# Optimization experiments

Measured on AMD Instinct MI355X. Metric: run time of the kernel, lower is better.

## Reference

```python
import jax, jax.numpy as jnp
import numpy as np

B, C, H, W, NH = 8, 256, 32, 32, 4  # batch, channels, height, width, heads


def groupnorm(x, w, b, eps=1e-5):
    # GroupNorm with 1 group: normalize over (C,H,W) per sample
    mu = x.mean(axis=(1, 2, 3), keepdims=True)
    var = x.var(axis=(1, 2, 3), keepdims=True)
    xn = (x - mu) * jax.lax.rsqrt(var + eps)
    return xn * w[None, :, None, None] + b[None, :, None, None]


def setup_inputs() -> dict:
    key = jax.random.key(0)
    ks = jax.random.split(key, 6)
    C4 = 4 * C
    s = lambda k, shape, scale: jax.random.normal(k, shape, jnp.float32) * scale
    return {
        "x": jax.random.normal(ks[0], (B, C, H, W), jnp.float32),
        "qkv_w": s(ks[1], (3 * C, C), 0.05),   # 1x1 conv, no bias
        "uh_w": s(ks[2], (C, C), 0.05),
        "uh_b": jnp.zeros((C,), jnp.float32),
        "n1_w": jnp.ones((C,), jnp.float32),
        "n1_b": jnp.zeros((C,), jnp.float32),
        "n2_w": jnp.ones((C,), jnp.float32),
        "n2_b": jnp.zeros((C,), jnp.float32),
        "f1_w": s(ks[3], (C4, C), 0.05),
        "f1_b": jnp.zeros((C4,), jnp.float32),
        "f2_w": s(ks[4], (C, C4), 0.05),
        "f2_b": jnp.zeros((C,), jnp.float32),
        # torch inits these to 0; use nonzero values so both branches contribute
        "gamma_attn": jnp.array(0.5, jnp.float32),
        "gamma_ffn": jnp.array(0.5, jnp.float32),
    }


def reference(x, qkv_w, uh_w, uh_b, n1_w, n1_b, n2_w, n2_b,
              f1_w, f1_b, f2_w, f2_b, gamma_attn, gamma_ffn):
    Bx, Cx, Hx, Wx = x.shape
    N = Hx * Wx
    dk = Cx // NH
    # --- attention branch (eval mode: DropPath is identity) ---
    xn = groupnorm(x, n1_w, n1_b).reshape(Bx, Cx, N)
    qkv = jnp.einsum('oc,bcn->bon', qkv_w, xn)          # 1x1 conv == channel matmul
    q, k, v = [t.reshape(Bx, NH, dk, N) for t in jnp.split(qkv, 3, axis=1)]
    scores = jnp.einsum('bhdi,bhdj->bhij', q, k) / np.float32(np.sqrt(dk))
    attn = jax.nn.softmax(scores, axis=-1)               # [B,H,N,N]
    out = jnp.einsum('bhij,bhdj->bhdi', attn, v).reshape(Bx, Cx, N)
    uh = jnp.einsum('oc,bcn->bon', uh_w, out) + uh_b[None, :, None]
    x2 = x + gamma_attn * uh.reshape(Bx, Cx, Hx, Wx)
    # --- FFN branch ---
    h = groupnorm(x2, n2_w, n2_b).reshape(Bx, Cx, N)
    h = jax.nn.silu(jnp.einsum('oc,bcn->bon', f1_w, h) + f1_b[None, :, None])
    h = jnp.einsum('oc,bcn->bon', f2_w, h) + f2_b[None, :, None]
    return x2 + gamma_ffn * h.reshape(Bx, Cx, Hx, Wx)
```

## Files before the change

kernel.cpp:

```cpp
#include <hip/hip_runtime.h>
#include <math.h>

#define Bsz 8
#define Cch 256
#define Nsp 1024
#define NHd 4
#define QS  0.18033688011112042f

using bf16x8  = __attribute__((ext_vector_type(8))) short;
using f32x4   = __attribute__((ext_vector_type(4))) float;
using ushort8 = __attribute__((ext_vector_type(8))) unsigned short;
#define MFMA(a,b,c) __builtin_amdgcn_mfma_f32_16x16x32_bf16(a,b,c,0,0,0)

__device__ inline unsigned short f2bf(float f) {
    unsigned int u = __float_as_uint(f);
    u = u + 0x7fffu + ((u >> 16) & 1u);
    return (unsigned short)(u >> 16);
}
__device__ inline float bf2f(unsigned short u) {
    return __uint_as_float((unsigned int)u << 16);
}
__device__ inline unsigned int cvtpk(float lo, float hi) {
    unsigned int r;
    asm("v_cvt_pk_bf16_f32 %0, %1, %2" : "=v"(r) : "v"(lo), "v"(hi));
    return r;
}

__global__ __launch_bounds__(256) void wconv_gn(const float* __restrict__ a, const float* __restrict__ b,
                                                const float* __restrict__ c, const float* __restrict__ d,
                                                unsigned short* __restrict__ o,
                                                const float* __restrict__ x,
                                                float* __restrict__ part) {
    if (blockIdx.x < 3072) {
        size_t i = (size_t)blockIdx.x * 256 + threadIdx.x;
        float v;
        if (i < 196608) v = a[i];
        else if (i < 262144) v = b[i - 196608];
        else if (i < 524288) v = c[i - 262144];
        else v = d[i - 524288];
        o[i] = f2bf(v);
        return;
    }
    int blk = blockIdx.x - 3072;
    int bb = blk >> 6;
    const float* xb = x + (size_t)bb * (Cch * Nsp) + (size_t)(blk & 63) * 4096;
    int t = threadIdx.x;
    float s = 0.f, s2 = 0.f;
    for (int i = t; i < 4096; i += 256) { float v = xb[i]; s += v; s2 += v * v; }
    __shared__ float sh[256], sh2[256];
    sh[t] = s; sh2[t] = s2; __syncthreads();
    for (int off = 128; off; off >>= 1) {
        if (t < off) { sh[t] += sh[t + off]; sh2[t] += sh2[t + off]; }
        __syncthreads();
    }
    if (t == 0) { part[blk * 2] = sh[0]; part[blk * 2 + 1] = sh2[0]; }
}

__global__ __launch_bounds__(256) void gn_apply_t(const float* __restrict__ x,
                                                  const float* __restrict__ part, int npart,
                                                  const float* __restrict__ w,
                                                  const float* __restrict__ bb,
                                                  unsigned short* __restrict__ out_cl) {
    int b = blockIdx.z, c0 = blockIdx.y * 64, n0 = blockIdx.x * 64;
    __shared__ float tile[64][65];
    __shared__ float smu, srs;
    int t = threadIdx.x;
    if (t < 64) {
        float s = 0.f, s2 = 0.f;
        for (int u = t; u < npart; u += 64) {
            s += part[(b * npart + u) * 2]; s2 += part[(b * npart + u) * 2 + 1];
        }
        for (int m = 1; m < 64; m <<= 1) { s += __shfl_xor(s, m); s2 += __shfl_xor(s2, m); }
        if (t == 0) {
            float inv_n = 1.f / (Cch * Nsp);
            float mu = s * inv_n;
            float var = s2 * inv_n - mu * mu;
            smu = mu; srs = rsqrtf(var + 1e-5f);
        }
    }
    const float* xb = x + ((size_t)b * Cch + c0) * Nsp + n0;
    for (int i = 0; i < 16; i++) {
        int e = t + i * 256; int r = e >> 6, c = e & 63;
        tile[r][c] = xb[(size_t)r * Nsp + c];
    }
    __syncthreads();
    float mu = smu, rs = srs;
    unsigned short* ob = out_cl + ((size_t)b * Nsp + n0) * Cch + c0;
    for (int i = 0; i < 16; i++) {
        int e = t + i * 256; int nr = e >> 6, nc = e & 63;
        int c = c0 + nc;
        float v = (tile[nc][nr] - mu) * rs * w[c] + bb[c];
        ob[(size_t)nr * Cch + nc] = f2bf(v);
    }
}

template<int K, int KL, int NFRAG>
__global__ __launch_bounds__(256, 4) void gemm_lds(
        const unsigned short* __restrict__ W,
        const unsigned short* __restrict__ Xcl,
        int epi, int act, int xmode,
        unsigned short* __restrict__ ocl, int Ocl, int ocol0,
        unsigned short* __restrict__ orm,
        float* __restrict__ pf, const float* __restrict__ res,
        unsigned short* __restrict__ x2cl,
        const float* __restrict__ gamma, const float* __restrict__ bias,
        float* __restrict__ part,
        const float* __restrict__ gnpart,
        const float* __restrict__ gnw, const float* __restrict__ gnb) {
    static_assert(KL == 256, "K-loop hardcoded for KL=256 (8 steps)");
    constexpr int NTILE = NFRAG * 16;
    constexpr int CPR = KL / 8;
    constexpr int TOTCH = NTILE * CPR;
    int z = blockIdx.z, nb = blockIdx.x, ob = blockIdx.y;
    int b = (epi == 4) ? (z & 7) : z;
    int kofs = (epi == 4) ? (z >> 3) * KL : 0;
    int t = threadIdx.x, w = t >> 6, l = t & 63, lg = l >> 4, lm = l & 15;
    __shared__ unsigned short Xs[NTILE * KL];
    __shared__ float sgn[2];
    const unsigned short* Xb = Xcl + ((size_t)b * Nsp + nb * NTILE) * K + kofs;
    int o_base = ob * 256 + w * 64;
    const unsigned short* Wp = W + (size_t)(o_base + lm) * K + kofs + 8 * lg;
    int m8 = lm & 7;

    bf16x8 wA0, wA1, wA2, wA3, wB0, wB1, wB2, wB3, wC0, wC1, wC2, wC3;
    #define WL(d0, d1, d2, d3, ks_) do {                                   \
        d0 = *(const bf16x8*)(Wp + (size_t)(0)      + (ks_) * 32);         \
        d1 = *(const bf16x8*)(Wp + (size_t)16 * K   + (ks_) * 32);         \
        d2 = *(const bf16x8*)(Wp + (size_t)32 * K   + (ks_) * 32);         \
        d3 = *(const bf16x8*)(Wp + (size_t)48 * K   + (ks_) * 32);         \
    } while (0)
    WL(wA0, wA1, wA2, wA3, 0);
    WL(wB0, wB1, wB2, wB3, 1);

    if (xmode == 0) {
        #pragma unroll
        for (int i = 0; i < TOTCH / 256; i++) {
            int c = i * 256 + t;
            int n = c / CPR, s = c % CPR;
            int gc = s ^ (n & 7);
            *(bf16x8*)&Xs[c * 8] = *(const bf16x8*)(Xb + (size_t)n * K + gc * 8);
        }
    } else {
        if (t < 64) {
            float s = gnpart[(b * 64 + t) * 2], s2 = gnpart[(b * 64 + t) * 2 + 1];
            for (int m = 1; m < 64; m <<= 1) { s += __shfl_xor(s, m); s2 += __shfl_xor(s2, m); }
            if (t == 0) {
                float inv_n = 1.f / (Cch * Nsp);
                float mu = s * inv_n;
                float var = s2 * inv_n - mu * mu;
                sgn[0] = mu; sgn[1] = rsqrtf(var + 1e-5f);
            }
        }
        __syncthreads();
        float mu = sgn[0], rs = sgn[1];
        #pragma unroll
        for (int i = 0; i < TOTCH / 256; i++) {
            int c = i * 256 + t;
            int n = c / CPR, s = c % CPR;
            int gc = s ^ (n & 7);
            ushort8 xv = *(const ushort8*)(Xb + (size_t)n * K + gc * 8);
            f32x4 w0 = *(const f32x4*)(gnw + gc * 8);
            f32x4 w1 = *(const f32x4*)(gnw + gc * 8 + 4);
            f32x4 b0 = *(const f32x4*)(gnb + gc * 8);
            f32x4 b1 = *(const f32x4*)(gnb + gc * 8 + 4);
            ushort8 rr;
            #pragma unroll
            for (int j = 0; j < 4; j++) {
                rr[j]     = f2bf((bf2f(xv[j])     - mu) * rs * w0[j] + b0[j]);
                rr[4 + j] = f2bf((bf2f(xv[4 + j]) - mu) * rs * w1[j] + b1[j]);
            }
            *(ushort8*)&Xs[c * 8] = rr;
        }
    }
    __syncthreads();

    f32x4 acc[4][NFRAG] = {};
    #define KS(w0_, w1_, w2_, w3_, ks_) do {                               \
        _Pragma("unroll")                                                  \
        for (int nf = 0; nf < NFRAG; nf++) {                               \
            int slot = ((ks_) * 4 + lg) ^ m8;                              \
            bf16x8 xf = *(const bf16x8*)&Xs[((nf * 16 + lm) * CPR + slot) * 8]; \
            acc[0][nf] = MFMA(w0_, xf, acc[0][nf]);                        \
            acc[1][nf] = MFMA(w1_, xf, acc[1][nf]);                        \
            acc[2][nf] = MFMA(w2_, xf, acc[2][nf]);                        \
            acc[3][nf] = MFMA(w3_, xf, acc[3][nf]);                        \
        }                                                                  \
    } while (0)
    WL(wC0, wC1, wC2, wC3, 2); KS(wA0, wA1, wA2, wA3, 0);
    WL(wA0, wA1, wA2, wA3, 3); KS(wB0, wB1, wB2, wB3, 1);
    WL(wB0, wB1, wB2, wB3, 4); KS(wC0, wC1, wC2, wC3, 2);
    WL(wC0, wC1, wC2, wC3, 5); KS(wA0, wA1, wA2, wA3, 3);
    WL(wA0, wA1, wA2, wA3, 6); KS(wB0, wB1, wB2, wB3, 4);
    WL(wB0, wB1, wB2, wB3, 7); KS(wC0, wC1, wC2, wC3, 5);
    KS(wA0, wA1, wA2, wA3, 6);
    KS(wB0, wB1, wB2, wB3, 7);
    #undef WL
    #undef KS

    if (epi == 0) {
        if (act == 3 && o_base >= 512) {
            #pragma unroll
            for (int nf = 0; nf < NFRAG; nf++) {
                int n = nb * NTILE + nf * 16 + lm;
                #pragma unroll
                for (int q = 0; q < 4; q++)
                    #pragma unroll
                    for (int r = 0; r < 4; r++) {
                        int o = o_base + q * 16 + 4 * lg + r - 512;
                        orm[((size_t)b * Cch + o) * Nsp + n] = f2bf(acc[q][nf][r]);
                    }
            }
        } else {
            float sc = (act == 3 && o_base < 256) ? QS : 1.f;
            #pragma unroll
            for (int nf = 0; nf < NFRAG; nf++) {
                int n = nb * NTILE + nf * 16 + lm;
                unsigned short* dst = ocl + ((size_t)b * Nsp + n) * Ocl + ocol0 + o_base + 4 * lg;
                #pragma unroll
                for (int q = 0; q < 4; q++) {
                    unsigned long long pk = 0;
                    #pragma unroll
                    for (int r = 0; r < 4; r++) {
                        int o = o_base + q * 16 + 4 * lg + r;
                        float v = acc[q][nf][r];
                        if (bias) v += bias[o];
                        if (act == 1) v = v / (1.f + __expf(-v));
                        else v *= sc;
                        pk |= (unsigned long long)f2bf(v) << (16 * r);
                    }
                    *(unsigned long long*)(dst + q * 16) = pk;
                }
            }
        }
    } else if (epi == 2) {
        float g = gamma[0];
        float ps = 0.f, ps2 = 0.f;
        #pragma unroll
        for (int nf = 0; nf < NFRAG; nf++) {
            int n = nb * NTILE + nf * 16 + lm;
            unsigned short* cdst = x2cl + ((size_t)b * Nsp + n) * Cch + o_base + 4 * lg;
            #pragma unroll
            for (int q = 0; q < 4; q++) {
                unsigned long long pk = 0;
                #pragma unroll
                for (int r = 0; r < 4; r++) {
                    int o = o_base + q * 16 + 4 * lg + r;
                    float v = acc[q][nf][r];
                    if (bias) v += bias[o];
                    size_t idx = ((size_t)b * Cch + o) * Nsp + n;
                    float ov = res[idx] + g * v;
                    pf[idx] = ov;
                    ps += ov; ps2 += ov * ov;
                    pk |= (unsigned long long)f2bf(ov) << (16 * r);
                }
                *(unsigned long long*)(cdst + q * 16) = pk;
            }
        }
        float* rsh  = (float*)&Xs[0];
        float* rsh2 = rsh + 256;
        __syncthreads();
        rsh[t] = ps; rsh2[t] = ps2; __syncthreads();
        for (int off = 128; off; off >>= 1) {
            if (t < off) { rsh[t] += rsh[t + off]; rsh2[t] += rsh2[t + off]; }
            __syncthreads();
        }
        if (t == 0) {
            int slot = b * gridDim.x + nb;
            part[slot * 2] = rsh[0]; part[slot * 2 + 1] = rsh2[0];
        }
    } else {
        #pragma unroll
        for (int nf = 0; nf < NFRAG; nf++) {
            int n = nb * NTILE + nf * 16 + lm;
            #pragma unroll
            for (int q = 0; q < 4; q++) {
                unsigned long long pk = 0;
                #pragma unroll
                for (int r = 0; r < 4; r++)
                    pk |= (unsigned long long)f2bf(acc[q][nf][r]) << (16 * r);
                unsigned short* dst = &orm[((size_t)z * Cch + o_base + q * 16 + 4 * lg) * Nsp + n];
                dst[0] = (unsigned short)(pk);
                dst[Nsp] = (unsigned short)(pk >> 16);
                dst[2 * Nsp] = (unsigned short)(pk >> 32);
                dst[3 * Nsp] = (unsigned short)(pk >> 48);
            }
        }
    }
}

__global__ __launch_bounds__(256) void attn_mfma8(const unsigned short* __restrict__ qk,
                                                  const unsigned short* __restrict__ v,
                                                  unsigned short* __restrict__ Opart,
                                                  float* __restrict__ lpart) {
    int L = blockIdx.x;
    int xcd = L & 7, jj = L >> 3;
    int g = xcd * 4 + (jj >> 5);
    int m = jj & 31;
    int h = g & 3, b = g >> 2;
    int ib = m & 7, sp = m >> 3;
    int t = threadIdx.x, w = t >> 6, l = t & 63, lg = l >> 4, lm = l & 15;
    __shared__ unsigned short KVs[2][4096];
    __shared__ unsigned short P[4][2][32][36];
    int i0 = ib * 128 + w * 32;
    int j0 = sp * 256;
    const unsigned short* qb = qk + ((size_t)b * Nsp + i0 + lm) * 512 + h * 64 + 8 * lg;
    bf16x8 qf00 = *(const bf16x8*)(qb);
    bf16x8 qf01 = *(const bf16x8*)(qb + 32);
    bf16x8 qf10 = *(const bf16x8*)(qb + 16 * 512);
    bf16x8 qf11 = *(const bf16x8*)(qb + 16 * 512 + 32);

    const unsigned short *gs0, *gs1;
    int lo0, lo1;
    size_t gstep;
    if (t < 128) {
        int c = 2 * t;
        int r = c >> 3, s = c & 7, swr = r & 7;
        const unsigned short* rowp = qk + ((size_t)b * Nsp + j0 + r) * 512 + 256 + h * 64;
        gs0 = rowp + ((s ^ swr) * 8);
        gs1 = rowp + (((s + 1) ^ swr) * 8);
        lo0 = c * 8; lo1 = lo0 + 8;
        gstep = (size_t)32 * 512;
    } else {
        int c = 2 * (t - 128);
        int d = c >> 2, s = c & 3, swd = d & 3;
        const unsigned short* rowp = v + ((size_t)b * Cch + h * 64 + d) * Nsp + j0;
        gs0 = rowp + ((s ^ swd) * 8);
        gs1 = rowp + (((s + 1) ^ swd) * 8);
        lo0 = 2048 + c * 8; lo1 = lo0 + 8;
        gstep = 32;
    }
    int cA = (lg ^ (lm & 7)) * 8;
    int cB = ((4 + lg) ^ (lm & 7)) * 8;
    int cV = (lg ^ (lm & 3)) * 8;

    f32x4 O00 = {}, O01 = {}, O02 = {}, O03 = {};
    f32x4 O10 = {}, O11 = {}, O12 = {}, O13 = {};
    float ls0 = 0.f, ls1 = 0.f;
    bf16x8 sg0, sg1;

    #define ISSUE(tile) do { sg0 = *(const bf16x8*)(gs0 + (size_t)(tile) * gstep); \
                             sg1 = *(const bf16x8*)(gs1 + (size_t)(tile) * gstep); } while (0)
    #define WRITE(bu) do { *(bf16x8*)&KVs[bu][lo0] = sg0; \
                           *(bf16x8*)&KVs[bu][lo1] = sg1; } while (0)
    #define QKC8(bu, pb) do {                                                     \
        const unsigned short* Ka = KVs[bu] + lm * 64;                             \
        const unsigned short* Kc = KVs[bu] + (16 + lm) * 64;                      \
        bf16x8 k00 = *(const bf16x8*)(Ka + cA);                                   \
        bf16x8 k01 = *(const bf16x8*)(Ka + cB);                                   \
        bf16x8 k10 = *(const bf16x8*)(Kc + cA);                                   \
        bf16x8 k11 = *(const bf16x8*)(Kc + cB);                                   \
        f32x4 s00 = {}, s01 = {}, s10 = {}, s11 = {};                             \
        s00 = MFMA(k00, qf00, s00); s00 = MFMA(k01, qf01, s00);                   \
        s01 = MFMA(k00, qf10, s01); s01 = MFMA(k01, qf11, s01);                   \
        s10 = MFMA(k10, qf00, s10); s10 = MFMA(k11, qf01, s10);                   \
        s11 = MFMA(k10, qf10, s11); s11 = MFMA(k11, qf11, s11);                   \
        float p0, p1, p2, p3; uint2 pk;                                           \
        p0 = exp2f(s00[0]); p1 = exp2f(s00[1]); p2 = exp2f(s00[2]); p3 = exp2f(s00[3]); \
        ls0 += (p0 + p1) + (p2 + p3);                                             \
        pk.x = cvtpk(p0, p1); pk.y = cvtpk(p2, p3);                               \
        *(uint2*)&P[w][pb][lm][4 * lg] = pk;                                      \
        p0 = exp2f(s01[0]); p1 = exp2f(s01[1]); p2 = exp2f(s01[2]); p3 = exp2f(s01[3]); \
        ls1 += (p0 + p1) + (p2 + p3);                                             \
        pk.x = cvtpk(p0, p1); pk.y = cvtpk(p2, p3);                               \
        *(uint2*)&P[w][pb][16 + lm][4 * lg] = pk;                                 \
        p0 = exp2f(s10[0]); p1 = exp2f(s10[1]); p2 = exp2f(s10[2]); p3 = exp2f(s10[3]); \
        ls0 += (p0 + p1) + (p2 + p3);                                             \
        pk.x = cvtpk(p0, p1); pk.y = cvtpk(p2, p3);                               \
        *(uint2*)&P[w][pb][lm][16 + 4 * lg] = pk;                                 \
        p0 = exp2f(s11[0]); p1 = exp2f(s11[1]); p2 = exp2f(s11[2]); p3 = exp2f(s11[3]); \
        ls1 += (p0 + p1) + (p2 + p3);                                             \
        pk.x = cvtpk(p0, p1); pk.y = cvtpk(p2, p3);                               \
        *(uint2*)&P[w][pb][16 + lm][16 + 4 * lg] = pk;                            \
    } while (0)
    #define PVC8(bu, pb) do {                                                     \
        bf16x8 pa0 = *(const bf16x8*)&P[w][pb][lm][8 * lg];                       \
        bf16x8 pa1 = *(const bf16x8*)&P[w][pb][16 + lm][8 * lg];                  \
        const unsigned short* Vl = KVs[bu] + 2048;                                \
        bf16x8 v0 = *(const bf16x8*)(Vl + lm * 32 + cV);                          \
        bf16x8 v1 = *(const bf16x8*)(Vl + (16 + lm) * 32 + cV);                   \
        bf16x8 v2 = *(const bf16x8*)(Vl + (32 + lm) * 32 + cV);                   \
        bf16x8 v3 = *(const bf16x8*)(Vl + (48 + lm) * 32 + cV);                   \
        O00 = MFMA(v0, pa0, O00); O10 = MFMA(v0, pa1, O10);                       \
        O01 = MFMA(v1, pa0, O01); O11 = MFMA(v1, pa1, O11);                       \
        O02 = MFMA(v2, pa0, O02); O12 = MFMA(v2, pa1, O12);                       \
        O03 = MFMA(v3, pa0, O03); O13 = MFMA(v3, pa1, O13);                       \
    } while (0)

    ISSUE(0); WRITE(0); __syncthreads();
    ISSUE(1);
    QKC8(0, 0);
    __syncthreads();
    WRITE(1);
    __syncthreads();
    #pragma unroll
    for (int tt = 1; tt < 8; tt++) {
        if (tt < 7) ISSUE(tt + 1);
        QKC8(tt & 1, tt & 1);
        PVC8((tt - 1) & 1, (tt - 1) & 1);
        __syncthreads();
        if (tt < 7) WRITE((tt + 1) & 1);
        __syncthreads();
    }
    PVC8(1, 1);
    #undef ISSUE
    #undef WRITE
    #undef QKC8
    #undef PVC8

    ls0 += __shfl_xor(ls0, 16); ls0 += __shfl_xor(ls0, 32);
    ls1 += __shfl_xor(ls1, 16); ls1 += __shfl_xor(ls1, 32);
    if (lg == 0) {
        float* lp = lpart + (((size_t)sp * Bsz + b) * NHd + h) * Nsp + i0 + lm;
        lp[0] = ls0;
        lp[16] = ls1;
    }
    unsigned short* ob0 = Opart + (((size_t)sp * Bsz + b) * Nsp + i0 + lm) * Cch + h * 64 + 4 * lg;
    unsigned short* ob1 = ob0 + (size_t)16 * Cch;
    uint2 pk;
    #define STO(dt, Oa, Ob_) \
        pk.x = cvtpk(Oa[0], Oa[1]); pk.y = cvtpk(Oa[2], Oa[3]); \
        *(uint2*)(ob0 + dt * 16) = pk; \
        pk.x = cvtpk(Ob_[0], Ob_[1]); pk.y = cvtpk(Ob_[2], Ob_[3]); \
        *(uint2*)(ob1 + dt * 16) = pk;
    STO(0, O00, O10) STO(1, O01, O11) STO(2, O02, O12) STO(3, O03, O13)
    #undef STO
}

__global__ __launch_bounds__(256) void attn_combine4(const unsigned short* __restrict__ Op,
                                                     const float* __restrict__ lp,
                                                     unsigned short* __restrict__ attno) {
    int idx = blockIdx.x * 256 + threadIdx.x;
    int b = idx >> 15;
    int i = (idx >> 5) & 1023;
    int c0 = (idx & 31) * 8;
    int h = c0 >> 6;
    size_t e = (size_t)(idx >> 5) * 256 + c0;
    const size_t SPO = (size_t)Bsz * Nsp * Cch;
    float acc[8] = {};
    float lsum = 0.f;
    #pragma unroll
    for (int sp = 0; sp < 4; sp++) {
        ushort8 o = *(const ushort8*)(Op + sp * SPO + e);
        #pragma unroll
        for (int j = 0; j < 8; j++) acc[j] += bf2f(o[j]);
        lsum += lp[(((size_t)sp * Bsz + b) * NHd + h) * Nsp + i];
    }
    float inv = 1.f / lsum;
    ushort8 r;
    #pragma unroll
    for (int j = 0; j < 8; j++) r[j] = f2bf(acc[j] * inv);
    *(ushort8*)(attno + e) = r;
}

__global__ __launch_bounds__(256) void f2_fin(const unsigned short* __restrict__ p,
                                              const float* __restrict__ x2,
                                              const float* __restrict__ bias,
                                              const float* __restrict__ gamma,
                                              float* __restrict__ out) {
    int idx = blockIdx.x * 256 + threadIdx.x;
    size_t e = (size_t)idx * 8;
    int o = (int)((e >> 10) & 255);
    const size_t SPO = (size_t)Bsz * Cch * Nsp;
    float acc[8] = {};
    #pragma unroll
    for (int sp = 0; sp < 4; sp++) {
        ushort8 v = *(const ushort8*)(p + sp * SPO + e);
        #pragma unroll
        for (int j = 0; j < 8; j++) acc[j] += bf2f(v[j]);
    }
    float g = gamma[0], bo = bias[o];
    f32x4 x0 = *(const f32x4*)(x2 + e);
    f32x4 x1 = *(const f32x4*)(x2 + e + 4);
    f32x4 r0, r1;
    #pragma unroll
    for (int j = 0; j < 4; j++) {
        r0[j] = x0[j] + g * (acc[j] + bo);
        r1[j] = x1[j] + g * (acc[4 + j] + bo);
    }
    *(f32x4*)(out + e) = r0;
    *(f32x4*)(out + e + 4) = r1;
}

extern "C" void kernel_launch(void* const* d_in, const int* in_sizes, int n_in,
                              void* d_out, int out_size, void* d_ws, size_t ws_size,
                              hipStream_t stream) {
    const float* x      = (const float*)d_in[0];
    const float* qkv_w  = (const float*)d_in[1];
    const float* uh_w   = (const float*)d_in[2];
    const float* uh_b   = (const float*)d_in[3];
    const float* n1_w   = (const float*)d_in[4];
    const float* n1_b   = (const float*)d_in[5];
    const float* n2_w   = (const float*)d_in[6];
    const float* n2_b   = (const float*)d_in[7];
    const float* f1_w   = (const float*)d_in[8];
    const float* f1_b   = (const float*)d_in[9];
    const float* f2_w   = (const float*)d_in[10];
    const float* f2_b   = (const float*)d_in[11];
    const float* g_attn = (const float*)d_in[12];
    const float* g_ffn  = (const float*)d_in[13];
    float* out = (float*)d_out;
    char* ws = (char*)d_ws;

    float*          part1   = (float*)(ws + 1024);
    float*          part2   = (float*)(ws + 5120);
    unsigned short* wbf     = (unsigned short*)(ws + 16384);
    unsigned short* xn_cl   = (unsigned short*)(ws + 2097152);
    float*          lpart   = (float*)(ws + 2097152);
    unsigned short* praw_bf = (unsigned short*)(ws + 2097152);
    unsigned short* qk_cl   = (unsigned short*)(ws + 6291456);
    unsigned short* vbuf    = (unsigned short*)(ws + 14680064);
    unsigned short* x2cl    = (unsigned short*)(ws + 14680064);
    unsigned short* attno   = (unsigned short*)(ws + 18874368);
    unsigned short* Opart   = (unsigned short*)(ws + 23068672);
    float*          x2      = (float*)(ws + 23068672);
    unsigned short* h1_cl   = (unsigned short*)(ws + 31457280);

    unsigned short* wbf_qkv = wbf;
    unsigned short* wbf_uh  = wbf + 196608;
    unsigned short* wbf_f1  = wbf + 262144;
    unsigned short* wbf_f2  = wbf + 524288;

    wconv_gn<<<3584, 256, 0, stream>>>(qkv_w, uh_w, f1_w, f2_w, wbf, x, part1);

    gn_apply_t<<<dim3(16, 4, Bsz), 256, 0, stream>>>(x, part1, 64, n1_w, n1_b, xn_cl);
    gemm_lds<256, 256, 2><<<dim3(32, 3, Bsz), 256, 0, stream>>>(wbf_qkv, xn_cl, 0, 3, 0,
        qk_cl, 512, 0, vbuf, nullptr, nullptr, nullptr, nullptr, nullptr, nullptr,
        nullptr, nullptr, nullptr);
    attn_mfma8<<<1024, 256, 0, stream>>>(qk_cl, vbuf, Opart, lpart);
    attn_combine4<<<1024, 256, 0, stream>>>(Opart, lpart, attno);
    gemm_lds<256, 256, 1><<<dim3(64, 1, Bsz), 256, 0, stream>>>(wbf_uh, attno, 2, 0, 0,
        nullptr, 0, 0, nullptr, x2, x, x2cl, g_attn, uh_b, part2,
        nullptr, nullptr, nullptr);

    gemm_lds<256, 256, 2><<<dim3(32, 4, Bsz), 256, 0, stream>>>(wbf_f1, x2cl, 0, 1, 1,
        h1_cl, 1024, 0, nullptr, nullptr, nullptr, nullptr, nullptr, f1_b, nullptr,
        part2, n2_w, n2_b);
    gemm_lds<1024, 256, 2><<<dim3(32, 1, 32), 256, 0, stream>>>(wbf_f2, h1_cl, 4, 0, 0,
        nullptr, 0, 0, praw_bf, nullptr, nullptr, nullptr, nullptr, nullptr, nullptr,
        nullptr, nullptr, nullptr);
    f2_fin<<<1024, 256, 0, stream>>>(praw_bf, x2, f2_b, g_ffn, out);
}
```

Measured before the change: 128.2 us.

## Fuse attention combine into uh GEMM and replace f2 split-K with in-kernel K loop

The attention partial-combine step (summing four split outputs and dividing by the softmax denominators) moves into the load stage of the uh projection GEMM, which removes one kernel launch and one intermediate buffer. The f2 GEMM no longer uses split-K with a separate reduction kernel. It loops over all four K chunks inside one block, double-buffering the LDS tiles and prefetching the next chunk into registers, then applies bias, gamma and the residual directly in its epilogue. The f2 grid is four times smaller and occupancy is lowered to 2 blocks per CU, so parallelism drops in exchange for less memory traffic and fewer launches.

```diff
diff --git a/kernel.cpp b/kernel.cpp
--- a/kernel.cpp
+++ b/kernel.cpp
@@ -95,7 +95,7 @@
 }
 
 template<int K, int KL, int NFRAG>
-__global__ __launch_bounds__(256, 4) void gemm_lds(
+__global__ __launch_bounds__(256, (K > 256) ? 2 : 4) void gemm_lds(
         const unsigned short* __restrict__ W,
         const unsigned short* __restrict__ Xcl,
         int epi, int act, int xmode,
@@ -108,29 +108,31 @@
         const float* __restrict__ gnpart,
         const float* __restrict__ gnw, const float* __restrict__ gnb) {
     static_assert(KL == 256, "K-loop hardcoded for KL=256 (8 steps)");
+    constexpr int NK = K / KL;
     constexpr int NTILE = NFRAG * 16;
     constexpr int CPR = KL / 8;
     constexpr int TOTCH = NTILE * CPR;
-    int z = blockIdx.z, nb = blockIdx.x, ob = blockIdx.y;
-    int b = (epi == 4) ? (z & 7) : z;
-    int kofs = (epi == 4) ? (z >> 3) * KL : 0;
+    int b = blockIdx.z, nb = blockIdx.x, ob = blockIdx.y;
     int t = threadIdx.x, w = t >> 6, l = t & 63, lg = l >> 4, lm = l & 15;
-    __shared__ unsigned short Xs[NTILE * KL];
+    __shared__ unsigned short Xs[(NK > 1 ? 2 : 1) * NTILE * KL];
     __shared__ float sgn[2];
-    const unsigned short* Xb = Xcl + ((size_t)b * Nsp + nb * NTILE) * K + kofs;
+    unsigned short* Xs0 = Xs;
+    unsigned short* Xs1 = Xs + (NK > 1 ? NTILE * KL : 0);
+    const unsigned short* Xb = Xcl + ((size_t)b * Nsp + nb * NTILE) * K;
     int o_base = ob * 256 + w * 64;
-    const unsigned short* Wp = W + (size_t)(o_base + lm) * K + kofs + 8 * lg;
+    const unsigned short* Wp = W + (size_t)(o_base + lm) * K + 8 * lg;
     int m8 = lm & 7;
 
-    bf16x8 wA0, wA1, wA2, wA3, wB0, wB1, wB2, wB3, wC0, wC1, wC2, wC3;
-    #define WL(d0, d1, d2, d3, ks_) do {                                   \
-        d0 = *(const bf16x8*)(Wp + (size_t)(0)      + (ks_) * 32);         \
-        d1 = *(const bf16x8*)(Wp + (size_t)16 * K   + (ks_) * 32);         \
-        d2 = *(const bf16x8*)(Wp + (size_t)32 * K   + (ks_) * 32);         \
-        d3 = *(const bf16x8*)(Wp + (size_t)48 * K   + (ks_) * 32);         \
+    bf16x8 wr[3][4];
+    #define WLOAD(sl, g_) do {                                             \
+        const unsigned short* wp_ = Wp + ((g_) >> 3) * KL + ((g_) & 7) * 32; \
+        wr[sl][0] = *(const bf16x8*)(wp_);                                 \
+        wr[sl][1] = *(const bf16x8*)(wp_ + (size_t)16 * K);                \
+        wr[sl][2] = *(const bf16x8*)(wp_ + (size_t)32 * K);                \
+        wr[sl][3] = *(const bf16x8*)(wp_ + (size_t)48 * K);                \
     } while (0)
-    WL(wA0, wA1, wA2, wA3, 0);
-    WL(wB0, wB1, wB2, wB3, 1);
+    WLOAD(0, 0);
+    WLOAD(1, 1);
 
     if (xmode == 0) {
         #pragma unroll
@@ -138,9 +140,9 @@
             int c = i * 256 + t;
             int n = c / CPR, s = c % CPR;
             int gc = s ^ (n & 7);
-            *(bf16x8*)&Xs[c * 8] = *(const bf16x8*)(Xb + (size_t)n * K + gc * 8);
-        }
-    } else {
+            *(bf16x8*)&Xs0[c * 8] = *(const bf16x8*)(Xb + (size_t)n * K + gc * 8);
+        }
+    } else if (xmode == 1) {
         if (t < 64) {
             float s = gnpart[(b * 64 + t) * 2], s2 = gnpart[(b * 64 + t) * 2 + 1];
             for (int m = 1; m < 64; m <<= 1) { s += __shfl_xor(s, m); s2 += __shfl_xor(s2, m); }
@@ -169,33 +171,79 @@
                 rr[j]     = f2bf((bf2f(xv[j])     - mu) * rs * w0[j] + b0[j]);
                 rr[4 + j] = f2bf((bf2f(xv[4 + j]) - mu) * rs * w1[j] + b1[j]);
             }
-            *(ushort8*)&Xs[c * 8] = rr;
+            *(ushort8*)&Xs0[c * 8] = rr;
+        }
+    } else {
+        const size_t SPO = (size_t)Bsz * Nsp * Cch;
+        #pragma unroll
+        for (int i = 0; i < TOTCH / 256; i++) {
+            int c = i * 256 + t;
+            int n = c / CPR, s = c % CPR;
+            int gc = s ^ (n & 7);
+            const unsigned short* p0 = Xb + (size_t)n * K + gc * 8;
+            int h = gc >> 3;
+            int gn = nb * NTILE + n;
+            float a0[8] = {};
+            float lsum = 0.f;
+            #pragma unroll
+            for (int sp = 0; sp < 4; sp++) {
+                ushort8 ov = *(const ushort8*)(p0 + (size_t)sp * SPO);
+                #pragma unroll
+                for (int j = 0; j < 8; j++) a0[j] += bf2f(ov[j]);
+                lsum += gnpart[(((size_t)sp * Bsz + b) * NHd + h) * Nsp + gn];
+            }
+            float inv = 1.f / lsum;
+            ushort8 rr;
+            #pragma unroll
+            for (int j = 0; j < 8; j++) rr[j] = f2bf(a0[j] * inv);
+            *(ushort8*)&Xs0[c * 8] = rr;
         }
     }
     __syncthreads();
 
     f32x4 acc[4][NFRAG] = {};
-    #define KS(w0_, w1_, w2_, w3_, ks_) do {                               \
+    bf16x8 st[TOTCH / 256];
+    #define KSTEP(sl, s_, Xp) do {                                         \
         _Pragma("unroll")                                                  \
         for (int nf = 0; nf < NFRAG; nf++) {                               \
-            int slot = ((ks_) * 4 + lg) ^ m8;                              \
-            bf16x8 xf = *(const bf16x8*)&Xs[((nf * 16 + lm) * CPR + slot) * 8]; \
-            acc[0][nf] = MFMA(w0_, xf, acc[0][nf]);                        \
-            acc[1][nf] = MFMA(w1_, xf, acc[1][nf]);                        \
-            acc[2][nf] = MFMA(w2_, xf, acc[2][nf]);                        \
-            acc[3][nf] = MFMA(w3_, xf, acc[3][nf]);                        \
+            int slot = ((s_) * 4 + lg) ^ m8;                               \
+            bf16x8 xf = *(const bf16x8*)&(Xp)[((nf * 16 + lm) * CPR + slot) * 8]; \
+            acc[0][nf] = MFMA(wr[sl][0], xf, acc[0][nf]);                  \
+            acc[1][nf] = MFMA(wr[sl][1], xf, acc[1][nf]);                  \
+            acc[2][nf] = MFMA(wr[sl][2], xf, acc[2][nf]);                  \
+            acc[3][nf] = MFMA(wr[sl][3], xf, acc[3][nf]);                  \
         }                                                                  \
     } while (0)
-    WL(wC0, wC1, wC2, wC3, 2); KS(wA0, wA1, wA2, wA3, 0);
-    WL(wA0, wA1, wA2, wA3, 3); KS(wB0, wB1, wB2, wB3, 1);
-    WL(wB0, wB1, wB2, wB3, 4); KS(wC0, wC1, wC2, wC3, 2);
-    WL(wC0, wC1, wC2, wC3, 5); KS(wA0, wA1, wA2, wA3, 3);
-    WL(wA0, wA1, wA2, wA3, 6); KS(wB0, wB1, wB2, wB3, 4);
-    WL(wB0, wB1, wB2, wB3, 7); KS(wC0, wC1, wC2, wC3, 5);
-    KS(wA0, wA1, wA2, wA3, 6);
-    KS(wB0, wB1, wB2, wB3, 7);
-    #undef WL
-    #undef KS
+
+    #pragma unroll
+    for (int g = 0; g < 8 * NK; g++) {
+        const int r = g >> 3, s = g & 7;
+        if (NK > 1 && r + 1 < NK && s == 0) {
+            #pragma unroll
+            for (int i = 0; i < TOTCH / 256; i++) {
+                int c = i * 256 + t;
+                int n = c / CPR, sc = c % CPR;
+                int gc = sc ^ (n & 7);
+                st[i] = *(const bf16x8*)(Xb + (size_t)n * K + (r + 1) * KL + gc * 8);
+            }
+        }
+        if (g + 2 < 8 * NK) WLOAD((g + 2) % 3, g + 2);
+        {
+            const unsigned short* Xp = (r & 1) ? Xs1 : Xs0;
+            KSTEP(g % 3, s, Xp);
+        }
+        if (NK > 1 && r + 1 < NK && s == 6) {
+            unsigned short* dst = (r & 1) ? Xs0 : Xs1;
+            #pragma unroll
+            for (int i = 0; i < TOTCH / 256; i++) {
+                int c = i * 256 + t;
+                *(bf16x8*)&dst[c * 8] = st[i];
+            }
+        }
+        if (NK > 1 && r + 1 < NK && s == 7) __syncthreads();
+    }
+    #undef WLOAD
+    #undef KSTEP
 
     if (epi == 0) {
         if (act == 3 && o_base >= 512) {
@@ -269,20 +317,18 @@
             part[slot * 2] = rsh[0]; part[slot * 2 + 1] = rsh2[0];
         }
     } else {
+        float g = gamma[0];
         #pragma unroll
         for (int nf = 0; nf < NFRAG; nf++) {
             int n = nb * NTILE + nf * 16 + lm;
             #pragma unroll
             for (int q = 0; q < 4; q++) {
-                unsigned long long pk = 0;
                 #pragma unroll
-                for (int r = 0; r < 4; r++)
-                    pk |= (unsigned long long)f2bf(acc[q][nf][r]) << (16 * r);
-                unsigned short* dst = &orm[((size_t)z * Cch + o_base + q * 16 + 4 * lg) * Nsp + n];
-                dst[0] = (unsigned short)(pk);
-                dst[Nsp] = (unsigned short)(pk >> 16);
-                dst[2 * Nsp] = (unsigned short)(pk >> 32);
-                dst[3 * Nsp] = (unsigned short)(pk >> 48);
+                for (int r = 0; r < 4; r++) {
+                    int o = o_base + q * 16 + 4 * lg + r;
+                    size_t idx = ((size_t)b * Cch + o) * Nsp + n;
+                    pf[idx] = res[idx] + g * (acc[q][nf][r] + bias[o]);
+                }
             }
         }
     }
@@ -426,61 +472,6 @@
     #undef STO
 }
 
-__global__ __launch_bounds__(256) void attn_combine4(const unsigned short* __restrict__ Op,
-                                                     const float* __restrict__ lp,
-                                                     unsigned short* __restrict__ attno) {
-    int idx = blockIdx.x * 256 + threadIdx.x;
-    int b = idx >> 15;
-    int i = (idx >> 5) & 1023;
-    int c0 = (idx & 31) * 8;
-    int h = c0 >> 6;
-    size_t e = (size_t)(idx >> 5) * 256 + c0;
-    const size_t SPO = (size_t)Bsz * Nsp * Cch;
-    float acc[8] = {};
-    float lsum = 0.f;
-    #pragma unroll
-    for (int sp = 0; sp < 4; sp++) {
-        ushort8 o = *(const ushort8*)(Op + sp * SPO + e);
-        #pragma unroll
-        for (int j = 0; j < 8; j++) acc[j] += bf2f(o[j]);
-        lsum += lp[(((size_t)sp * Bsz + b) * NHd + h) * Nsp + i];
-    }
-    float inv = 1.f / lsum;
-    ushort8 r;
-    #pragma unroll
-    for (int j = 0; j < 8; j++) r[j] = f2bf(acc[j] * inv);
-    *(ushort8*)(attno + e) = r;
-}
-
-__global__ __launch_bounds__(256) void f2_fin(const unsigned short* __restrict__ p,
-                                              const float* __restrict__ x2,
-                                              const float* __restrict__ bias,
-                                              const float* __restrict__ gamma,
-                                              float* __restrict__ out) {
-    int idx = blockIdx.x * 256 + threadIdx.x;
-    size_t e = (size_t)idx * 8;
-    int o = (int)((e >> 10) & 255);
-    const size_t SPO = (size_t)Bsz * Cch * Nsp;
-    float acc[8] = {};
-    #pragma unroll
-    for (int sp = 0; sp < 4; sp++) {
-        ushort8 v = *(const ushort8*)(p + sp * SPO + e);
-        #pragma unroll
-        for (int j = 0; j < 8; j++) acc[j] += bf2f(v[j]);
-    }
-    float g = gamma[0], bo = bias[o];
-    f32x4 x0 = *(const f32x4*)(x2 + e);
-    f32x4 x1 = *(const f32x4*)(x2 + e + 4);
-    f32x4 r0, r1;
-    #pragma unroll
-    for (int j = 0; j < 4; j++) {
-        r0[j] = x0[j] + g * (acc[j] + bo);
-        r1[j] = x1[j] + g * (acc[4 + j] + bo);
-    }
-    *(f32x4*)(out + e) = r0;
-    *(f32x4*)(out + e + 4) = r1;
-}
-
 extern "C" void kernel_launch(void* const* d_in, const int* in_sizes, int n_in,
                               void* d_out, int out_size, void* d_ws, size_t ws_size,
                               hipStream_t stream) {
@@ -506,14 +497,12 @@
     unsigned short* wbf     = (unsigned short*)(ws + 16384);
     unsigned short* xn_cl   = (unsigned short*)(ws + 2097152);
     float*          lpart   = (float*)(ws + 2097152);
-    unsigned short* praw_bf = (unsigned short*)(ws + 2097152);
     unsigned short* qk_cl   = (unsigned short*)(ws + 6291456);
     unsigned short* vbuf    = (unsigned short*)(ws + 14680064);
     unsigned short* x2cl    = (unsigned short*)(ws + 14680064);
-    unsigned short* attno   = (unsigned short*)(ws + 18874368);
     unsigned short* Opart   = (unsigned short*)(ws + 23068672);
-    float*          x2      = (float*)(ws + 23068672);
     unsigned short* h1_cl   = (unsigned short*)(ws + 31457280);
+    float*          x2      = (float*)(ws + 50331648);
 
     unsigned short* wbf_qkv = wbf;
     unsigned short* wbf_uh  = wbf + 196608;
@@ -527,16 +516,14 @@
         qk_cl, 512, 0, vbuf, nullptr, nullptr, nullptr, nullptr, nullptr, nullptr,
         nullptr, nullptr, nullptr);
     attn_mfma8<<<1024, 256, 0, stream>>>(qk_cl, vbuf, Opart, lpart);
-    attn_combine4<<<1024, 256, 0, stream>>>(Opart, lpart, attno);
-    gemm_lds<256, 256, 1><<<dim3(64, 1, Bsz), 256, 0, stream>>>(wbf_uh, attno, 2, 0, 0,
+    gemm_lds<256, 256, 1><<<dim3(64, 1, Bsz), 256, 0, stream>>>(wbf_uh, Opart, 2, 0, 2,
         nullptr, 0, 0, nullptr, x2, x, x2cl, g_attn, uh_b, part2,
-        nullptr, nullptr, nullptr);
+        lpart, nullptr, nullptr);
 
     gemm_lds<256, 256, 2><<<dim3(32, 4, Bsz), 256, 0, stream>>>(wbf_f1, x2cl, 0, 1, 1,
         h1_cl, 1024, 0, nullptr, nullptr, nullptr, nullptr, nullptr, f1_b, nullptr,
         part2, n2_w, n2_b);
-    gemm_lds<1024, 256, 2><<<dim3(32, 1, 32), 256, 0, stream>>>(wbf_f2, h1_cl, 4, 0, 0,
-        nullptr, 0, 0, praw_bf, nullptr, nullptr, nullptr, nullptr, nullptr, nullptr,
+    gemm_lds<1024, 256, 2><<<dim3(32, 1, Bsz), 256, 0, stream>>>(wbf_f2, h1_cl, 5, 0, 0,
+        nullptr, 0, 0, nullptr, out, x2, nullptr, g_ffn, f2_b, nullptr,
         nullptr, nullptr, nullptr);
-    f2_fin<<<1024, 256, 0, stream>>>(praw_bf, x2, f2_b, g_ffn, out);
-}
+}
```

New measurement: 118.4 us. -7.6%, faster.

## Fuse GroupNorm apply into QKV GEMM and attention combine into out-proj GEMM

Applied to the files above, without the earlier changes.

Removes the separate gn_apply_t transpose kernel by having the QKV GEMM read fp32 x directly, normalize it with the GN1 statistics, and write bf16 into its LDS tile (xmode 3). It also removes the attn_combine4 kernel by having the output-projection GEMM sum the four split-K attention partials and divide by the softmax denominators while loading its X tile (xmode 2). Workspace offsets are rearranged so the buffers no longer alias. This saves two launches and the intermediate round trips to global memory. In exchange the GEMM prologues do more work: the xmode 3 path makes strided fp32 reads from x, and the combine step is repeated by each output-column block.

```diff
diff --git a/kernel.cpp b/kernel.cpp
--- a/kernel.cpp
+++ b/kernel.cpp
@@ -54,44 +54,6 @@
         __syncthreads();
     }
     if (t == 0) { part[blk * 2] = sh[0]; part[blk * 2 + 1] = sh2[0]; }
-}
-
-__global__ __launch_bounds__(256) void gn_apply_t(const float* __restrict__ x,
-                                                  const float* __restrict__ part, int npart,
-                                                  const float* __restrict__ w,
-                                                  const float* __restrict__ bb,
-                                                  unsigned short* __restrict__ out_cl) {
-    int b = blockIdx.z, c0 = blockIdx.y * 64, n0 = blockIdx.x * 64;
-    __shared__ float tile[64][65];
-    __shared__ float smu, srs;
-    int t = threadIdx.x;
-    if (t < 64) {
-        float s = 0.f, s2 = 0.f;
-        for (int u = t; u < npart; u += 64) {
-            s += part[(b * npart + u) * 2]; s2 += part[(b * npart + u) * 2 + 1];
-        }
-        for (int m = 1; m < 64; m <<= 1) { s += __shfl_xor(s, m); s2 += __shfl_xor(s2, m); }
-        if (t == 0) {
-            float inv_n = 1.f / (Cch * Nsp);
-            float mu = s * inv_n;
-            float var = s2 * inv_n - mu * mu;
-            smu = mu; srs = rsqrtf(var + 1e-5f);
-        }
-    }
-    const float* xb = x + ((size_t)b * Cch + c0) * Nsp + n0;
-    for (int i = 0; i < 16; i++) {
-        int e = t + i * 256; int r = e >> 6, c = e & 63;
-        tile[r][c] = xb[(size_t)r * Nsp + c];
-    }
-    __syncthreads();
-    float mu = smu, rs = srs;
-    unsigned short* ob = out_cl + ((size_t)b * Nsp + n0) * Cch + c0;
-    for (int i = 0; i < 16; i++) {
-        int e = t + i * 256; int nr = e >> 6, nc = e & 63;
-        int c = c0 + nc;
-        float v = (tile[nc][nr] - mu) * rs * w[c] + bb[c];
-        ob[(size_t)nr * Cch + nc] = f2bf(v);
-    }
 }
 
 template<int K, int KL, int NFRAG>
@@ -140,7 +102,7 @@
             int gc = s ^ (n & 7);
             *(bf16x8*)&Xs[c * 8] = *(const bf16x8*)(Xb + (size_t)n * K + gc * 8);
         }
-    } else {
+    } else if (xmode == 1) {
         if (t < 64) {
             float s = gnpart[(b * 64 + t) * 2], s2 = gnpart[(b * 64 + t) * 2 + 1];
             for (int m = 1; m < 64; m <<= 1) { s += __shfl_xor(s, m); s2 += __shfl_xor(s2, m); }
@@ -170,6 +132,58 @@
                 rr[4 + j] = f2bf((bf2f(xv[4 + j]) - mu) * rs * w1[j] + b1[j]);
             }
             *(ushort8*)&Xs[c * 8] = rr;
+        }
+    } else if (xmode == 2) {
+        const size_t SPO = (size_t)Bsz * Nsp * Cch;
+        #pragma unroll
+        for (int i = 0; i < TOTCH / 256; i++) {
+            int c = i * 256 + t;
+            int n = c / CPR, s = c % CPR;
+            int gc = s ^ (n & 7);
+            const unsigned short* p0 = Xb + (size_t)n * K + gc * 8;
+            int h = gc >> 3;
+            int gn = nb * NTILE + n;
+            float a0[8] = {};
+            float lsum = 0.f;
+            #pragma unroll
+            for (int sp = 0; sp < 4; sp++) {
+                ushort8 ov = *(const ushort8*)(p0 + (size_t)sp * SPO);
+                #pragma unroll
+                for (int j = 0; j < 8; j++) a0[j] += bf2f(ov[j]);
+                lsum += gnpart[(((size_t)sp * Bsz + b) * NHd + h) * Nsp + gn];
+            }
+            float inv = 1.f / lsum;
+            ushort8 rr;
+            #pragma unroll
+            for (int j = 0; j < 8; j++) rr[j] = f2bf(a0[j] * inv);
+            *(ushort8*)&Xs[c * 8] = rr;
+        }
+    } else {
+        if (t < 64) {
+            float s = gnpart[(b * 64 + t) * 2], s2 = gnpart[(b * 64 + t) * 2 + 1];
+            for (int m = 1; m < 64; m <<= 1) { s += __shfl_xor(s, m); s2 += __shfl_xor(s2, m); }
+            if (t == 0) {
+                float inv_n = 1.f / (Cch * Nsp);
+                float mu = s * inv_n;
+                float var = s2 * inv_n - mu * mu;
+                sgn[0] = mu; sgn[1] = rsqrtf(var + 1e-5f);
+            }
+        }
+        __syncthreads();
+        float mu = sgn[0], rs = sgn[1];
+        int n = t & 31;
+        #pragma unroll
+        for (int i = 0; i < 4; i++) {
+            int G = i * 8 + (t >> 5);
+            const float* xr = res + ((size_t)b * Cch + G * 8) * Nsp + (size_t)nb * NTILE + n;
+            ushort8 rr;
+            #pragma unroll
+            for (int j = 0; j < 8; j++) {
+                float val = xr[(size_t)j * Nsp];
+                rr[j] = f2bf((val - mu) * rs * gnw[G * 8 + j] + gnb[G * 8 + j]);
+            }
+            int slot = G ^ (n & 7);
+            *(ushort8*)&Xs[(n * 32 + slot) * 8] = rr;
         }
     }
     __syncthreads();
@@ -286,6 +300,35 @@
             }
         }
     }
+}
+
+__global__ __launch_bounds__(256) void f2_fin(const unsigned short* __restrict__ p,
+                                              const float* __restrict__ x2,
+                                              const float* __restrict__ bias,
+                                              const float* __restrict__ gamma,
+                                              float* __restrict__ out) {
+    int idx = blockIdx.x * 256 + threadIdx.x;
+    size_t e = (size_t)idx * 8;
+    int o = (int)((e >> 10) & 255);
+    const size_t SPO = (size_t)Bsz * Cch * Nsp;
+    float acc[8] = {};
+    #pragma unroll
+    for (int sp = 0; sp < 4; sp++) {
+        ushort8 v = *(const ushort8*)(p + sp * SPO + e);
+        #pragma unroll
+        for (int j = 0; j < 8; j++) acc[j] += bf2f(v[j]);
+    }
+    float g = gamma[0], bo = bias[o];
+    f32x4 x0 = *(const f32x4*)(x2 + e);
+    f32x4 x1 = *(const f32x4*)(x2 + e + 4);
+    f32x4 r0, r1;
+    #pragma unroll
+    for (int j = 0; j < 4; j++) {
+        r0[j] = x0[j] + g * (acc[j] + bo);
+        r1[j] = x1[j] + g * (acc[4 + j] + bo);
+    }
+    *(f32x4*)(out + e) = r0;
+    *(f32x4*)(out + e + 4) = r1;
 }
 
 __global__ __launch_bounds__(256) void attn_mfma8(const unsigned short* __restrict__ qk,
@@ -426,61 +469,6 @@
     #undef STO
 }
 
-__global__ __launch_bounds__(256) void attn_combine4(const unsigned short* __restrict__ Op,
-                                                     const float* __restrict__ lp,
-                                                     unsigned short* __restrict__ attno) {
-    int idx = blockIdx.x * 256 + threadIdx.x;
-    int b = idx >> 15;
-    int i = (idx >> 5) & 1023;
-    int c0 = (idx & 31) * 8;
-    int h = c0 >> 6;
-    size_t e = (size_t)(idx >> 5) * 256 + c0;
-    const size_t SPO = (size_t)Bsz * Nsp * Cch;
-    float acc[8] = {};
-    float lsum = 0.f;
-    #pragma unroll
-    for (int sp = 0; sp < 4; sp++) {
-        ushort8 o = *(const ushort8*)(Op + sp * SPO + e);
-        #pragma unroll
-        for (int j = 0; j < 8; j++) acc[j] += bf2f(o[j]);
-        lsum += lp[(((size_t)sp * Bsz + b) * NHd + h) * Nsp + i];
-    }
-    float inv = 1.f / lsum;
-    ushort8 r;
-    #pragma unroll
-    for (int j = 0; j < 8; j++) r[j] = f2bf(acc[j] * inv);
-    *(ushort8*)(attno + e) = r;
-}
-
-__global__ __launch_bounds__(256) void f2_fin(const unsigned short* __restrict__ p,
-                                              const float* __restrict__ x2,
-                                              const float* __restrict__ bias,
-                                              const float* __restrict__ gamma,
-                                              float* __restrict__ out) {
-    int idx = blockIdx.x * 256 + threadIdx.x;
-    size_t e = (size_t)idx * 8;
-    int o = (int)((e >> 10) & 255);
-    const size_t SPO = (size_t)Bsz * Cch * Nsp;
-    float acc[8] = {};
-    #pragma unroll
-    for (int sp = 0; sp < 4; sp++) {
-        ushort8 v = *(const ushort8*)(p + sp * SPO + e);
-        #pragma unroll
-        for (int j = 0; j < 8; j++) acc[j] += bf2f(v[j]);
-    }
-    float g = gamma[0], bo = bias[o];
-    f32x4 x0 = *(const f32x4*)(x2 + e);
-    f32x4 x1 = *(const f32x4*)(x2 + e + 4);
-    f32x4 r0, r1;
-    #pragma unroll
-    for (int j = 0; j < 4; j++) {
-        r0[j] = x0[j] + g * (acc[j] + bo);
-        r1[j] = x1[j] + g * (acc[4 + j] + bo);
-    }
-    *(f32x4*)(out + e) = r0;
-    *(f32x4*)(out + e + 4) = r1;
-}
-
 extern "C" void kernel_launch(void* const* d_in, const int* in_sizes, int n_in,
                               void* d_out, int out_size, void* d_ws, size_t ws_size,
                               hipStream_t stream) {
@@ -504,16 +492,14 @@
     float*          part1   = (float*)(ws + 1024);
     float*          part2   = (float*)(ws + 5120);
     unsigned short* wbf     = (unsigned short*)(ws + 16384);
-    unsigned short* xn_cl   = (unsigned short*)(ws + 2097152);
     float*          lpart   = (float*)(ws + 2097152);
-    unsigned short* praw_bf = (unsigned short*)(ws + 2097152);
     unsigned short* qk_cl   = (unsigned short*)(ws + 6291456);
     unsigned short* vbuf    = (unsigned short*)(ws + 14680064);
     unsigned short* x2cl    = (unsigned short*)(ws + 14680064);
-    unsigned short* attno   = (unsigned short*)(ws + 18874368);
     unsigned short* Opart   = (unsigned short*)(ws + 23068672);
-    float*          x2      = (float*)(ws + 23068672);
-    unsigned short* h1_cl   = (unsigned short*)(ws + 31457280);
+    float*          x2      = (float*)(ws + 50331648);
+    unsigned short* praw_bf = (unsigned short*)(ws + 67108864);
+    unsigned short* h1_cl   = (unsigned short*)(ws + 100663296);
 
     unsigned short* wbf_qkv = wbf;
     unsigned short* wbf_uh  = wbf + 196608;
@@ -522,15 +508,14 @@
 
     wconv_gn<<<3584, 256, 0, stream>>>(qkv_w, uh_w, f1_w, f2_w, wbf, x, part1);
 
-    gn_apply_t<<<dim3(16, 4, Bsz), 256, 0, stream>>>(x, part1, 64, n1_w, n1_b, xn_cl);
-    gemm_lds<256, 256, 2><<<dim3(32, 3, Bsz), 256, 0, stream>>>(wbf_qkv, xn_cl, 0, 3, 0,
-        qk_cl, 512, 0, vbuf, nullptr, nullptr, nullptr, nullptr, nullptr, nullptr,
-        nullptr, nullptr, nullptr);
+    gemm_lds<256, 256, 2><<<dim3(32, 3, Bsz), 256, 0, stream>>>(wbf_qkv,
+        (const unsigned short*)x, 0, 3, 3,
+        qk_cl, 512, 0, vbuf, nullptr, x, nullptr, nullptr, nullptr, nullptr,
+        part1, n1_w, n1_b);
     attn_mfma8<<<1024, 256, 0, stream>>>(qk_cl, vbuf, Opart, lpart);
-    attn_combine4<<<1024, 256, 0, stream>>>(Opart, lpart, attno);
-    gemm_lds<256, 256, 1><<<dim3(64, 1, Bsz), 256, 0, stream>>>(wbf_uh, attno, 2, 0, 0,
+    gemm_lds<256, 256, 1><<<dim3(64, 1, Bsz), 256, 0, stream>>>(wbf_uh, Opart, 2, 0, 2,
         nullptr, 0, 0, nullptr, x2, x, x2cl, g_attn, uh_b, part2,
-        nullptr, nullptr, nullptr);
+        lpart, nullptr, nullptr);
 
     gemm_lds<256, 256, 2><<<dim3(32, 4, Bsz), 256, 0, stream>>>(wbf_f1, x2cl, 0, 1, 1,
         h1_cl, 1024, 0, nullptr, nullptr, nullptr, nullptr, nullptr, f1_b, nullptr,
```

Result: faster. 121.2 us (-5.4%).
